# Kernel optimization log

Measured on AMD Instinct MI355X. Metric: run time of the kernel, lower is better.

The kernel has to match this reference:

```python
import jax, jax.numpy as jnp
import numpy as np

D_MODEL = 1024
D_Q = 1024
D_V = 1024


def setup_inputs() -> dict:
    key = jax.random.key(0)
    k0, k1, k2, k3 = jax.random.split(key, 4)
    embedding_word = jax.random.normal(k0, (4, 2048, D_MODEL), dtype=jnp.float32)
    # nn.Linear weights are [out, in]; we store transposed [in, out] for x @ W
    s = 1.0 / np.sqrt(D_MODEL)
    w_q = jax.random.uniform(k1, (D_MODEL, D_Q), jnp.float32, -s, s)
    w_k = jax.random.uniform(k2, (D_MODEL, D_Q), jnp.float32, -s, s)
    w_v = jax.random.uniform(k3, (D_MODEL, D_V), jnp.float32, -s, s)
    return {"embedding_word": embedding_word, "w_q": w_q, "w_k": w_k, "w_v": w_v}


def reference(embedding_word, w_q, w_k, w_v):
    # q,k: [B,T,d_q]; v: [B,T,d_v]
    q = embedding_word @ w_q
    k = embedding_word @ w_k
    v = embedding_word @ w_v
    scores = jnp.einsum("btd,bsd->bts", q, k)  # [B,T,T]
    T = scores.shape[-1]
    causal = jnp.tril(jnp.ones((T, T), dtype=bool))  # True = keep
    masked = jnp.where(causal, scores, -jnp.inf)
    weights = jax.nn.softmax(masked / jnp.sqrt(jnp.float32(D_Q)), axis=-1)
    return jnp.einsum("bts,bsv->btv", weights, v)
```

## Files before the change

### kernel.cpp

```cpp
#include <hip/hip_runtime.h>
#include <cstdint>

typedef __bf16 bf16_t;
typedef __attribute__((ext_vector_type(8))) __bf16 bf16x8;
typedef __attribute__((ext_vector_type(4))) __bf16 bf16x4;
typedef __attribute__((ext_vector_type(4))) float f32x4;

#define AS1 __attribute__((address_space(1)))
#define AS3 __attribute__((address_space(3)))

template <typename OutT>
__global__ __launch_bounds__(256)
void gemm_nt(const bf16_t* __restrict__ A, const bf16_t* __restrict__ B,
             OutT* __restrict__ C, int K, int lda, int ldb, int ldc)
{
  const int bm = blockIdx.y, bn = blockIdx.x;
  const int m0 = bm * 128, n0 = bn * 128;

  __shared__ bf16_t As[2][128 * 64];
  __shared__ bf16_t Bs[2][128 * 64];

  const int tid = threadIdx.x;
  const int wave = tid >> 6, lane = tid & 63;
  const int lm = lane & 15, qd = lane >> 4;
  const int wm = (wave >> 1) * 64, wn = (wave & 1) * 64;

  const int rowl = lane >> 3;
  const int q = (lane & 7) ^ rowl;
  const bf16_t* Abase = A + (long)(m0 + wave * 8 + rowl) * lda + q * 8;
  const bf16_t* Bbase = B + (long)(n0 + wave * 8 + rowl) * ldb + q * 8;
  const int woff = wave * 512;

  auto stage = [&](int k0, int b) {
#pragma unroll
    for (int i = 0; i < 4; i++) {
      __builtin_amdgcn_global_load_lds((const AS1 void*)(Abase + (long)i * 32 * lda + k0),
                                       (AS3 void*)(As[b] + woff + i * 2048), 16, 0, 0);
      __builtin_amdgcn_global_load_lds((const AS1 void*)(Bbase + (long)i * 32 * ldb + k0),
                                       (AS3 void*)(Bs[b] + woff + i * 2048), 16, 0, 0);
    }
  };

  f32x4 acc[4][4] = {};

  stage(0, 0);
  int buf = 0;
  for (int k0 = 0; k0 < K; k0 += 64) {
    __syncthreads();
    if (k0 + 64 < K) stage(k0 + 64, buf ^ 1);
#pragma unroll
    for (int s = 0; s < 2; s++) {
      bf16x8 aF[4], bF[4];
#pragma unroll
      for (int i = 0; i < 4; i++) {
        const int r = wm + i * 16 + lm;
        aF[i] = *(const bf16x8*)&As[buf][r * 64 + (((s * 4 + qd) ^ (lm & 7)) << 3)];
      }
#pragma unroll
      for (int j = 0; j < 4; j++) {
        const int r = wn + j * 16 + lm;
        bF[j] = *(const bf16x8*)&Bs[buf][r * 64 + (((s * 4 + qd) ^ (lm & 7)) << 3)];
      }
#pragma unroll
      for (int i = 0; i < 4; i++)
#pragma unroll
        for (int j = 0; j < 4; j++)
          acc[i][j] = __builtin_amdgcn_mfma_f32_16x16x32_bf16(aF[i], bF[j], acc[i][j], 0, 0, 0);
    }
    buf ^= 1;
  }

#pragma unroll
  for (int i = 0; i < 4; i++) {
    const int row = m0 + wm + i * 16 + qd * 4;
#pragma unroll
    for (int j = 0; j < 4; j++) {
      const int col = n0 + wn + j * 16 + lm;
#pragma unroll
      for (int r = 0; r < 4; r++)
        C[(long)(row + r) * ldc + col] = (OutT)acc[i][j][r];
    }
  }
}

template <typename OutT>
__global__ __launch_bounds__(256)
void gemm_ntc(const bf16_t* __restrict__ A, const bf16_t* __restrict__ B,
              OutT* __restrict__ C, int K, int lda, int ldb, int ldc,
              long sA, long sB, long sC, int causal, int kLimit)
{
  int bm = blockIdx.y;
  const int bn = blockIdx.x;
  if (kLimit) bm = gridDim.y - 1 - bm;
  if (causal && bn > bm) return;
  A += (long)blockIdx.z * sA;
  B += (long)blockIdx.z * sB;
  C += (long)blockIdx.z * sC;
  const int m0 = bm * 128, n0 = bn * 128;
  int Keff = K;
  if (kLimit) { const int kl = (bm + 1) * 128; if (kl < Keff) Keff = kl; }

  __shared__ bf16_t As[2][128 * 64];
  __shared__ bf16_t Bs[2][128 * 64];

  const int tid = threadIdx.x;
  const int wave = tid >> 6, lane = tid & 63;
  const int lm = lane & 15, qd = lane >> 4;
  const int wm = (wave >> 1) * 64, wn = (wave & 1) * 64;

  const int rowl = lane >> 3;
  const int q = (lane & 7) ^ rowl;
  const bf16_t* Abase = A + (long)(m0 + wave * 8 + rowl) * lda + q * 8;
  const bf16_t* Bbase = B + (long)(n0 + wave * 8 + rowl) * ldb + q * 8;
  const int woff = wave * 512;

  auto stage = [&](int k0, int b) {
#pragma unroll
    for (int i = 0; i < 4; i++) {
      __builtin_amdgcn_global_load_lds((const AS1 void*)(Abase + (long)i * 32 * lda + k0),
                                       (AS3 void*)(As[b] + woff + i * 2048), 16, 0, 0);
      __builtin_amdgcn_global_load_lds((const AS1 void*)(Bbase + (long)i * 32 * ldb + k0),
                                       (AS3 void*)(Bs[b] + woff + i * 2048), 16, 0, 0);
    }
  };

  f32x4 acc[4][4] = {};

  stage(0, 0);
  int buf = 0;
  for (int k0 = 0; k0 < Keff; k0 += 64) {
    __syncthreads();
    if (k0 + 64 < Keff) stage(k0 + 64, buf ^ 1);
#pragma unroll
    for (int s = 0; s < 2; s++) {
      bf16x8 aF[4], bF[4];
#pragma unroll
      for (int i = 0; i < 4; i++) {
        const int r = wm + i * 16 + lm;
        aF[i] = *(const bf16x8*)&As[buf][r * 64 + (((s * 4 + qd) ^ (lm & 7)) << 3)];
      }
#pragma unroll
      for (int j = 0; j < 4; j++) {
        const int r = wn + j * 16 + lm;
        bF[j] = *(const bf16x8*)&Bs[buf][r * 64 + (((s * 4 + qd) ^ (lm & 7)) << 3)];
      }
#pragma unroll
      for (int i = 0; i < 4; i++)
#pragma unroll
        for (int j = 0; j < 4; j++)
          acc[i][j] = __builtin_amdgcn_mfma_f32_16x16x32_bf16(aF[i], bF[j], acc[i][j], 0, 0, 0);
    }
    buf ^= 1;
  }

#pragma unroll
  for (int i = 0; i < 4; i++) {
    const int row = m0 + wm + i * 16 + qd * 4;
#pragma unroll
    for (int j = 0; j < 4; j++) {
      const int col = n0 + wn + j * 16 + lm;
#pragma unroll
      for (int r = 0; r < 4; r++)
        C[(long)(row + r) * ldc + col] = (OutT)acc[i][j][r];
    }
  }
}

__global__ __launch_bounds__(256)
void prep(const float* __restrict__ X, bf16_t* __restrict__ Xb,
          const float* __restrict__ wq, const float* __restrict__ wk,
          const float* __restrict__ wv, bf16_t* __restrict__ WT)
{
  const int b = blockIdx.x;
  if (b < 8192) {
    const int i = b * 256 + threadIdx.x;
    const float4 f = ((const float4*)X)[i];
    bf16x4 o = {(bf16_t)f.x, (bf16_t)f.y, (bf16_t)f.z, (bf16_t)f.w};
    ((bf16x4*)Xb)[i] = o;
    return;
  }
  const int wid = b - 8192;
  const int z = wid >> 10;
  const int t = wid & 1023;
  const int tix = t & 31, tiy = t >> 5;
  const float* W = (z == 0) ? wq : (z == 1) ? wk : wv;
  bf16_t* O = WT + (long)z * 1024 * 1024;

  __shared__ float tile[32][33];
  const int x = threadIdx.x & 31, y0 = threadIdx.x >> 5;
#pragma unroll
  for (int r = 0; r < 4; r++) {
    const int y = y0 + r * 8;
    tile[y][x] = W[(long)(tiy * 32 + y) * 1024 + (tix * 32 + x)];
  }
  __syncthreads();
#pragma unroll
  for (int r = 0; r < 4; r++) {
    const int y = y0 + r * 8;
    O[(long)(tix * 32 + y) * 1024 + (tiy * 32 + x)] = (bf16_t)tile[x][y];
  }
}

__global__ __launch_bounds__(256)
void softmax_causal(bf16_t* __restrict__ S)
{
  const int row = blockIdx.x;
  const int t = row & 2047;
  const int kend = ((t >> 7) + 1) << 7;
  bf16_t* Sr = S + (long)row * 2048;
  const int base = threadIdx.x * 8;

  uint4 u = {0, 0, 0, 0};
  if (base <= t) u = *(const uint4*)(Sr + base);
  const unsigned short* up = (const unsigned short*)&u;
  float v[8];
  float m = -3.0e38f;
#pragma unroll
  for (int j = 0; j < 8; j++) {
    const float x = __uint_as_float(((unsigned)up[j]) << 16);
    v[j] = (base + j <= t) ? x : -3.0e38f;
    m = fmaxf(m, v[j]);
  }
#pragma unroll
  for (int off = 32; off > 0; off >>= 1) m = fmaxf(m, __shfl_xor(m, off));
  __shared__ float redm[4], redl[4];
  const int wave = threadIdx.x >> 6, lane = threadIdx.x & 63;
  if (lane == 0) redm[wave] = m;
  __syncthreads();
  m = fmaxf(fmaxf(redm[0], redm[1]), fmaxf(redm[2], redm[3]));

  float p[8], l = 0.f;
#pragma unroll
  for (int j = 0; j < 8; j++) {
    p[j] = (base + j <= t) ? __expf((v[j] - m) * 0.03125f) : 0.f;
    l += p[j];
  }
#pragma unroll
  for (int off = 32; off > 0; off >>= 1) l += __shfl_xor(l, off);
  if (lane == 0) redl[wave] = l;
  __syncthreads();
  l = (redl[0] + redl[1]) + (redl[2] + redl[3]);
  const float rl = 1.0f / l;

  if (base < kend) {
    uint4 w;
    unsigned* wp = (unsigned*)&w;
#pragma unroll
    for (int h = 0; h < 4; h++) {
      bf16_t a = (bf16_t)(p[2 * h] * rl);
      bf16_t b = (bf16_t)(p[2 * h + 1] * rl);
      wp[h] = (unsigned)__builtin_bit_cast(unsigned short, a) |
              ((unsigned)__builtin_bit_cast(unsigned short, b) << 16);
    }
    *(uint4*)(Sr + base) = w;
  }
}

extern "C" void kernel_launch(void* const* d_in, const int* in_sizes, int n_in,
                              void* d_out, int out_size, void* d_ws, size_t ws_size,
                              hipStream_t stream)
{
  const float* X  = (const float*)d_in[0];
  const float* Wq = (const float*)d_in[1];
  const float* Wk = (const float*)d_in[2];
  const float* Wv = (const float*)d_in[3];
  float* out = (float*)d_out;

  char* p = (char*)d_ws;
  bf16_t* QK = (bf16_t*)p;  p += (size_t)8192 * 2048 * 2;
  bf16_t* VT = (bf16_t*)p;  p += (size_t)1024 * 8192 * 2;
  bf16_t* WT = (bf16_t*)p;  p += (size_t)3072 * 1024 * 2;
  bf16_t* Xb = (bf16_t*)p;
  bf16_t* S  = (bf16_t*)p;

  prep<<<8192 + 3072, 256, 0, stream>>>(X, Xb, Wq, Wk, Wv, WT);
  gemm_nt<bf16_t><<<dim3(16, 64), 256, 0, stream>>>(
      Xb, WT, QK, 1024, 1024, 1024, 2048);
  gemm_nt<bf16_t><<<dim3(64, 8), 256, 0, stream>>>(
      WT + (long)2048 * 1024, Xb, VT, 1024, 1024, 1024, 8192);
  gemm_ntc<bf16_t><<<dim3(16, 16, 4), 256, 0, stream>>>(
      QK, QK + 1024, S, 1024, 2048, 2048, 2048,
      (long)2048 * 2048, (long)2048 * 2048, (long)2048 * 2048, 1, 0);
  softmax_causal<<<8192, 256, 0, stream>>>(S);
  gemm_ntc<float><<<dim3(8, 16, 4), 256, 0, stream>>>(
      S, VT, out, 2048, 2048, 8192, 1024,
      (long)2048 * 2048, 2048, (long)2048 * 1024, 0, 1);
}
```

Measured before the change: 248.7 us.

## Replace 128x128 GEMMs with 256x256 8-wave ping-pong pipelined GEMM

Replaces both GEMM kernels with a single 256x256-tile kernel that runs 512 threads (8 waves). Its K loop is split into four MFMA phases, with LDS fragment reads and async global->LDS loads interleaved between them, separated by explicit barriers and guarded by s_setprio. The larger tile is meant to raise arithmetic intensity and hide load latency behind MFMA work. The causal block granularity grows to 256, so the softmax kend changes to match and more masked work runs near the diagonal. Grids shrink sharply (e.g. 128 or 256 blocks), which risks underfilling the CUs and adds heavy register pressure from the 8x4 accumulator array.

```diff
diff --git a/kernel.cpp b/kernel.cpp
--- a/kernel.cpp
+++ b/kernel.cpp
@@ -9,85 +9,45 @@
 #define AS1 __attribute__((address_space(1)))
 #define AS3 __attribute__((address_space(3)))
 
+
+#define READ_AQ(slot, bb, qidx)                                                \
+  _Pragma("unroll")                                                            \
+  for (int il = 0; il < 2; il++)                                               \
+    _Pragma("unroll")                                                          \
+    for (int s2 = 0; s2 < 2; s2++) {                                           \
+      const int r_ = wr * 128 + ((qidx) * 2 + il) * 16 + lm;                   \
+      aQ[slot][il * 2 + s2] =                                                  \
+        *(const bf16x8*)&As[bb][r_ * 64 + (((s2 * 4 + qd) ^ (lm & 7)) << 3)];  \
+    }
+
+#define READ_B(pi_, bb)                                                        \
+  _Pragma("unroll")                                                            \
+  for (int j = 0; j < 4; j++)                                                  \
+    _Pragma("unroll")                                                          \
+    for (int s2 = 0; s2 < 2; s2++) {                                           \
+      const int r_ = wc * 64 + j * 16 + lm;                                    \
+      bS[pi_][j * 2 + s2] =                                                    \
+        *(const bf16x8*)&Bs[bb][r_ * 64 + (((s2 * 4 + qd) ^ (lm & 7)) << 3)];  \
+    }
+
+#define MFMA_PH(p, slot, pi_)                                                  \
+  __builtin_amdgcn_s_setprio(1);                                               \
+  _Pragma("unroll")                                                            \
+  for (int il = 0; il < 2; il++)                                               \
+    _Pragma("unroll")                                                          \
+    for (int j = 0; j < 4; j++)                                                \
+      _Pragma("unroll")                                                        \
+      for (int s2 = 0; s2 < 2; s2++)                                           \
+        acc[(p) * 2 + il][j] = __builtin_amdgcn_mfma_f32_16x16x32_bf16(        \
+            aQ[slot][il * 2 + s2], bS[pi_][j * 2 + s2],                        \
+            acc[(p) * 2 + il][j], 0, 0, 0);                                    \
+  __builtin_amdgcn_s_setprio(0);
+
 template <typename OutT>
-__global__ __launch_bounds__(256)
-void gemm_nt(const bf16_t* __restrict__ A, const bf16_t* __restrict__ B,
-             OutT* __restrict__ C, int K, int lda, int ldb, int ldc)
-{
-  const int bm = blockIdx.y, bn = blockIdx.x;
-  const int m0 = bm * 128, n0 = bn * 128;
-
-  __shared__ bf16_t As[2][128 * 64];
-  __shared__ bf16_t Bs[2][128 * 64];
-
-  const int tid = threadIdx.x;
-  const int wave = tid >> 6, lane = tid & 63;
-  const int lm = lane & 15, qd = lane >> 4;
-  const int wm = (wave >> 1) * 64, wn = (wave & 1) * 64;
-
-  const int rowl = lane >> 3;
-  const int q = (lane & 7) ^ rowl;
-  const bf16_t* Abase = A + (long)(m0 + wave * 8 + rowl) * lda + q * 8;
-  const bf16_t* Bbase = B + (long)(n0 + wave * 8 + rowl) * ldb + q * 8;
-  const int woff = wave * 512;
-
-  auto stage = [&](int k0, int b) {
-#pragma unroll
-    for (int i = 0; i < 4; i++) {
-      __builtin_amdgcn_global_load_lds((const AS1 void*)(Abase + (long)i * 32 * lda + k0),
-                                       (AS3 void*)(As[b] + woff + i * 2048), 16, 0, 0);
-      __builtin_amdgcn_global_load_lds((const AS1 void*)(Bbase + (long)i * 32 * ldb + k0),
-                                       (AS3 void*)(Bs[b] + woff + i * 2048), 16, 0, 0);
-    }
-  };
-
-  f32x4 acc[4][4] = {};
-
-  stage(0, 0);
-  int buf = 0;
-  for (int k0 = 0; k0 < K; k0 += 64) {
-    __syncthreads();
-    if (k0 + 64 < K) stage(k0 + 64, buf ^ 1);
-#pragma unroll
-    for (int s = 0; s < 2; s++) {
-      bf16x8 aF[4], bF[4];
-#pragma unroll
-      for (int i = 0; i < 4; i++) {
-        const int r = wm + i * 16 + lm;
-        aF[i] = *(const bf16x8*)&As[buf][r * 64 + (((s * 4 + qd) ^ (lm & 7)) << 3)];
-      }
-#pragma unroll
-      for (int j = 0; j < 4; j++) {
-        const int r = wn + j * 16 + lm;
-        bF[j] = *(const bf16x8*)&Bs[buf][r * 64 + (((s * 4 + qd) ^ (lm & 7)) << 3)];
-      }
-#pragma unroll
-      for (int i = 0; i < 4; i++)
-#pragma unroll
-        for (int j = 0; j < 4; j++)
-          acc[i][j] = __builtin_amdgcn_mfma_f32_16x16x32_bf16(aF[i], bF[j], acc[i][j], 0, 0, 0);
-    }
-    buf ^= 1;
-  }
-
-#pragma unroll
-  for (int i = 0; i < 4; i++) {
-    const int row = m0 + wm + i * 16 + qd * 4;
-#pragma unroll
-    for (int j = 0; j < 4; j++) {
-      const int col = n0 + wn + j * 16 + lm;
-#pragma unroll
-      for (int r = 0; r < 4; r++)
-        C[(long)(row + r) * ldc + col] = (OutT)acc[i][j][r];
-    }
-  }
-}
-
-template <typename OutT>
-__global__ __launch_bounds__(256)
-void gemm_ntc(const bf16_t* __restrict__ A, const bf16_t* __restrict__ B,
-              OutT* __restrict__ C, int K, int lda, int ldb, int ldc,
-              long sA, long sB, long sC, int causal, int kLimit)
+__global__ __launch_bounds__(512, 2)
+void gemm256(const bf16_t* __restrict__ A, const bf16_t* __restrict__ B,
+             OutT* __restrict__ C, int K, int lda, int ldb, int ldc,
+             long sA, long sB, long sC, int causal, int kLimit)
 {
   int bm = blockIdx.y;
   const int bn = blockIdx.x;
@@ -96,69 +56,90 @@
   A += (long)blockIdx.z * sA;
   B += (long)blockIdx.z * sB;
   C += (long)blockIdx.z * sC;
-  const int m0 = bm * 128, n0 = bn * 128;
+  const int m0 = bm * 256, n0 = bn * 256;
   int Keff = K;
-  if (kLimit) { const int kl = (bm + 1) * 128; if (kl < Keff) Keff = kl; }
-
-  __shared__ bf16_t As[2][128 * 64];
-  __shared__ bf16_t Bs[2][128 * 64];
+  if (kLimit) { const int kl = (bm + 1) * 256; if (kl < Keff) Keff = kl; }
+
+  __shared__ bf16_t As[2][256 * 64];
+  __shared__ bf16_t Bs[2][256 * 64];
 
   const int tid = threadIdx.x;
   const int wave = tid >> 6, lane = tid & 63;
   const int lm = lane & 15, qd = lane >> 4;
-  const int wm = (wave >> 1) * 64, wn = (wave & 1) * 64;
-
+  const int wr = wave >> 2, wc = wave & 3;
   const int rowl = lane >> 3;
   const int q = (lane & 7) ^ rowl;
   const bf16_t* Abase = A + (long)(m0 + wave * 8 + rowl) * lda + q * 8;
   const bf16_t* Bbase = B + (long)(n0 + wave * 8 + rowl) * ldb + q * 8;
   const int woff = wave * 512;
 
-  auto stage = [&](int k0, int b) {
-#pragma unroll
-    for (int i = 0; i < 4; i++) {
-      __builtin_amdgcn_global_load_lds((const AS1 void*)(Abase + (long)i * 32 * lda + k0),
-                                       (AS3 void*)(As[b] + woff + i * 2048), 16, 0, 0);
-      __builtin_amdgcn_global_load_lds((const AS1 void*)(Bbase + (long)i * 32 * ldb + k0),
-                                       (AS3 void*)(Bs[b] + woff + i * 2048), 16, 0, 0);
-    }
+  auto stgA = [&](int kt, int b, int h) {
+#pragma unroll
+    for (int i = 0; i < 2; i++)
+      __builtin_amdgcn_global_load_lds(
+          (const AS1 void*)(Abase + (long)(h * 128 + i * 64) * lda + kt),
+          (AS3 void*)(As[b] + h * 8192 + i * 4096 + woff), 16, 0, 0);
   };
-
-  f32x4 acc[4][4] = {};
-
-  stage(0, 0);
-  int buf = 0;
-  for (int k0 = 0; k0 < Keff; k0 += 64) {
-    __syncthreads();
-    if (k0 + 64 < Keff) stage(k0 + 64, buf ^ 1);
-#pragma unroll
-    for (int s = 0; s < 2; s++) {
-      bf16x8 aF[4], bF[4];
-#pragma unroll
-      for (int i = 0; i < 4; i++) {
-        const int r = wm + i * 16 + lm;
-        aF[i] = *(const bf16x8*)&As[buf][r * 64 + (((s * 4 + qd) ^ (lm & 7)) << 3)];
-      }
-#pragma unroll
-      for (int j = 0; j < 4; j++) {
-        const int r = wn + j * 16 + lm;
-        bF[j] = *(const bf16x8*)&Bs[buf][r * 64 + (((s * 4 + qd) ^ (lm & 7)) << 3)];
-      }
-#pragma unroll
-      for (int i = 0; i < 4; i++)
-#pragma unroll
-        for (int j = 0; j < 4; j++)
-          acc[i][j] = __builtin_amdgcn_mfma_f32_16x16x32_bf16(aF[i], bF[j], acc[i][j], 0, 0, 0);
-    }
-    buf ^= 1;
-  }
-
-#pragma unroll
-  for (int i = 0; i < 4; i++) {
-    const int row = m0 + wm + i * 16 + qd * 4;
+  auto stgB = [&](int kt, int b, int h) {
+#pragma unroll
+    for (int i = 0; i < 2; i++)
+      __builtin_amdgcn_global_load_lds(
+          (const AS1 void*)(Bbase + (long)(h * 128 + i * 64) * ldb + kt),
+          (AS3 void*)(Bs[b] + h * 8192 + i * 4096 + woff), 16, 0, 0);
+  };
+
+  f32x4 acc[8][4] = {};
+  bf16x8 aQ[2][4];
+  bf16x8 bS[2][8];
+
+  stgB(0, 0, 0);  stgB(0, 0, 1);  stgA(0, 0, 0);  stgA(0, 0, 1);
+  stgB(64, 1, 0); stgB(64, 1, 1); stgA(64, 1, 0); stgA(64, 1, 1);
+  asm volatile("s_waitcnt vmcnt(8)" ::: "memory");
+  __builtin_amdgcn_s_barrier();
+  READ_B(0, 0);
+  READ_AQ(0, 0, 0);
+  __builtin_amdgcn_s_barrier();
+
+  for (int k0 = 0; k0 < Keff; k0 += 128) {
+#pragma unroll
+    for (int tt = 0; tt < 2; tt++) {
+      const int kk = k0 + tt * 64;
+      const bool stg = (kk + 128 < Keff);
+      const bool nxt = (kk + 64 < Keff);
+      READ_AQ(1, tt, 1);
+      if (stg) stgB(kk + 128, tt, 0);
+      __builtin_amdgcn_s_barrier();
+      __builtin_amdgcn_sched_barrier(0);
+      MFMA_PH(0, 0, tt);
+      __builtin_amdgcn_s_barrier();
+      READ_AQ(0, tt, 2);
+      if (stg) stgB(kk + 128, tt, 1);
+      __builtin_amdgcn_s_barrier();
+      __builtin_amdgcn_sched_barrier(0);
+      MFMA_PH(1, 1, tt);
+      __builtin_amdgcn_s_barrier();
+      READ_AQ(1, tt, 3);
+      if (stg) asm volatile("s_waitcnt vmcnt(4)" ::: "memory");
+      else     asm volatile("s_waitcnt vmcnt(0)" ::: "memory");
+      __builtin_amdgcn_s_barrier();
+      __builtin_amdgcn_sched_barrier(0);
+      MFMA_PH(2, 0, tt);
+      __builtin_amdgcn_s_barrier();
+      if (nxt) { READ_B(tt ^ 1, tt ^ 1); READ_AQ(0, tt ^ 1, 0); }
+      if (stg) { stgA(kk + 128, tt, 0); stgA(kk + 128, tt, 1); }
+      __builtin_amdgcn_s_barrier();
+      __builtin_amdgcn_sched_barrier(0);
+      MFMA_PH(3, 1, tt);
+      __builtin_amdgcn_s_barrier();
+    }
+  }
+
+#pragma unroll
+  for (int i = 0; i < 8; i++) {
+    const int row = m0 + wr * 128 + i * 16 + qd * 4;
 #pragma unroll
     for (int j = 0; j < 4; j++) {
-      const int col = n0 + wn + j * 16 + lm;
+      const int col = n0 + wc * 64 + j * 16 + lm;
 #pragma unroll
       for (int r = 0; r < 4; r++)
         C[(long)(row + r) * ldc + col] = (OutT)acc[i][j][r];
@@ -206,7 +187,7 @@
 {
   const int row = blockIdx.x;
   const int t = row & 2047;
-  const int kend = ((t >> 7) + 1) << 7;
+  const int kend = ((t >> 8) + 1) << 8;
   bf16_t* Sr = S + (long)row * 2048;
   const int base = threadIdx.x * 8;
 
@@ -274,15 +255,15 @@
   bf16_t* S  = (bf16_t*)p;
 
   prep<<<8192 + 3072, 256, 0, stream>>>(X, Xb, Wq, Wk, Wv, WT);
-  gemm_nt<bf16_t><<<dim3(16, 64), 256, 0, stream>>>(
-      Xb, WT, QK, 1024, 1024, 1024, 2048);
-  gemm_nt<bf16_t><<<dim3(64, 8), 256, 0, stream>>>(
-      WT + (long)2048 * 1024, Xb, VT, 1024, 1024, 1024, 8192);
-  gemm_ntc<bf16_t><<<dim3(16, 16, 4), 256, 0, stream>>>(
+  gemm256<bf16_t><<<dim3(8, 32, 1), 512, 0, stream>>>(
+      Xb, WT, QK, 1024, 1024, 1024, 2048, 0, 0, 0, 0, 0);
+  gemm256<bf16_t><<<dim3(32, 4, 1), 512, 0, stream>>>(
+      WT + (long)2048 * 1024, Xb, VT, 1024, 1024, 1024, 8192, 0, 0, 0, 0, 0);
+  gemm256<bf16_t><<<dim3(8, 8, 4), 512, 0, stream>>>(
       QK, QK + 1024, S, 1024, 2048, 2048, 2048,
       (long)2048 * 2048, (long)2048 * 2048, (long)2048 * 2048, 1, 0);
   softmax_causal<<<8192, 256, 0, stream>>>(S);
-  gemm_ntc<float><<<dim3(8, 16, 4), 256, 0, stream>>>(
+  gemm256<float><<<dim3(4, 8, 4), 512, 0, stream>>>(
       S, VT, out, 2048, 2048, 8192, 1024,
       (long)2048 * 2048, 2048, (long)2048 * 1024, 0, 1);
 }
```

Measured after the change: 289.2 us. 16.3% more time.

## Add 256x256-tile 8-wave GEMM with phased pipeline for Q/K projection

Applied to the files above, without the earlier changes.

Adds a new 512-thread GEMM kernel that computes 256x256 output tiles, splitting each K-step into four phases that interleave LDS fragment reads, async global-to-LDS staging of the next tiles and MFMA bursts under raised priority. It replaces the 128x128 kernel for the fused Q/K projection only. The larger tile raises arithmetic intensity and cuts global traffic per FLOP. In exchange it uses 128 KB of LDS and many accumulator registers per thread, and launches only 256 blocks, which may leave some CUs idle.

```diff
diff --git a/kernel.cpp b/kernel.cpp
--- a/kernel.cpp
+++ b/kernel.cpp
@@ -166,6 +166,123 @@
   }
 }
 
+template <typename OutT>
+__global__ __launch_bounds__(512, 2)
+void gemm256(const bf16_t* __restrict__ A, const bf16_t* __restrict__ B,
+             OutT* __restrict__ C, int K, int lda, int ldb, int ldc)
+{
+  const int bm = blockIdx.y, bn = blockIdx.x;
+  const int m0 = bm * 256, n0 = bn * 256;
+
+  __shared__ bf16_t As[2][256 * 64];
+  __shared__ bf16_t Bs[2][256 * 64];
+
+  const int tid = threadIdx.x;
+  const int wave = tid >> 6, lane = tid & 63;
+  const int lm = lane & 15, qd = lane >> 4;
+  const int wr = wave >> 2, wc = wave & 3;
+  const int wch = wc >> 1, wcl = wc & 1;
+  const int rowl = lane >> 3;
+  const int q = (lane & 7) ^ rowl;
+  const int woff = wave * 512;
+
+  auto stgAc = [&](int kt, int b, int c) {
+    const int grow = m0 + ((c & 1) << 7) + ((c >> 1) << 6) + wave * 8 + rowl;
+    __builtin_amdgcn_global_load_lds(
+        (const AS1 void*)(A + (long)grow * lda + q * 8 + kt),
+        (AS3 void*)(As[b] + c * 4096 + woff), 16, 0, 0);
+  };
+  auto stgBc = [&](int kt, int b, int c) {
+    const int gn = n0 + ((c & 1) << 7) + ((wave >> 2) << 6) + ((c >> 1) << 5) +
+                   (wave & 3) * 8 + rowl;
+    __builtin_amdgcn_global_load_lds(
+        (const AS1 void*)(B + (long)gn * ldb + q * 8 + kt),
+        (AS3 void*)(Bs[b] + c * 4096 + woff), 16, 0, 0);
+  };
+
+  f32x4 acc[8][4] = {};
+
+#define PHASE256(p, d, dn, kk, stg1, stg2)                                     \
+  {                                                                            \
+    constexpr int mp = (p) >> 1, np = (p) & 1;                                 \
+    bf16x8 aF[4][2], bF[2][2];                                                 \
+    _Pragma("unroll")                                                          \
+    for (int mi = 0; mi < 4; mi++)                                             \
+      _Pragma("unroll")                                                        \
+      for (int s2 = 0; s2 < 2; s2++) {                                         \
+        const int r_ = (wr + 2 * mp) * 64 + mi * 16 + lm;                      \
+        aF[mi][s2] =                                                           \
+          *(const bf16x8*)&As[d][r_ * 64 + (((s2 * 4 + qd) ^ (lm & 7)) << 3)]; \
+      }                                                                        \
+    _Pragma("unroll")                                                          \
+    for (int nj = 0; nj < 2; nj++)                                             \
+      _Pragma("unroll")                                                        \
+      for (int s2 = 0; s2 < 2; s2++) {                                         \
+        const int r_ = (np * 2 + wch) * 64 + wcl * 32 + nj * 16 + lm;          \
+        bF[nj][s2] =                                                           \
+          *(const bf16x8*)&Bs[d][r_ * 64 + (((s2 * 4 + qd) ^ (lm & 7)) << 3)]; \
+      }                                                                        \
+    if ((p) == 0 && (stg1)) { stgAc((kk) + 64, dn, 2); stgAc((kk) + 64, dn, 3); } \
+    if ((p) == 1 && (stg1)) { stgBc((kk) + 64, dn, 2); stgBc((kk) + 64, dn, 3); } \
+    if ((p) == 2 && (stg2)) { stgAc((kk) + 128, d, 0); stgAc((kk) + 128, d, 1); } \
+    if ((p) == 3 && (stg2)) { stgBc((kk) + 128, d, 0); stgBc((kk) + 128, d, 1); } \
+    if ((p) == 3) {                                                            \
+      if (stg2) asm volatile("s_waitcnt vmcnt(4)" ::: "memory");               \
+      else      asm volatile("s_waitcnt vmcnt(0)" ::: "memory");               \
+    }                                                                          \
+    __builtin_amdgcn_s_barrier();                                              \
+    asm volatile("s_waitcnt lgkmcnt(0)" ::: "memory");                         \
+    __builtin_amdgcn_sched_barrier(0);                                         \
+    __builtin_amdgcn_s_setprio(1);                                             \
+    _Pragma("unroll")                                                          \
+    for (int mi = 0; mi < 4; mi++)                                             \
+      _Pragma("unroll")                                                        \
+      for (int nj = 0; nj < 2; nj++)                                           \
+        _Pragma("unroll")                                                      \
+        for (int s2 = 0; s2 < 2; s2++)                                         \
+          acc[mp * 4 + mi][np * 2 + nj] =                                      \
+              __builtin_amdgcn_mfma_f32_16x16x32_bf16(                         \
+                  aF[mi][s2], bF[nj][s2], acc[mp * 4 + mi][np * 2 + nj],       \
+                  0, 0, 0);                                                    \
+    __builtin_amdgcn_s_setprio(0);                                             \
+    __builtin_amdgcn_s_barrier();                                              \
+  }
+
+  stgAc(0, 0, 0); stgAc(0, 0, 1); stgAc(0, 0, 2); stgAc(0, 0, 3);
+  stgBc(0, 0, 0); stgBc(0, 0, 1); stgBc(0, 0, 2); stgBc(0, 0, 3);
+  stgAc(64, 1, 0); stgAc(64, 1, 1);
+  stgBc(64, 1, 0); stgBc(64, 1, 1);
+  asm volatile("s_waitcnt vmcnt(4)" ::: "memory");
+  __builtin_amdgcn_s_barrier();
+
+  for (int kk = 0; kk < K; kk += 128) {
+    const bool s1a = (kk + 64  < K);
+    const bool s2a = (kk + 128 < K);
+    const bool s2b = (kk + 192 < K);
+    PHASE256(0, 0, 1, kk, s1a, s2a)
+    PHASE256(1, 0, 1, kk, s1a, s2a)
+    PHASE256(2, 0, 1, kk, s1a, s2a)
+    PHASE256(3, 0, 1, kk, s1a, s2a)
+    PHASE256(0, 1, 0, kk + 64, s2a, s2b)
+    PHASE256(1, 1, 0, kk + 64, s2a, s2b)
+    PHASE256(2, 1, 0, kk + 64, s2a, s2b)
+    PHASE256(3, 1, 0, kk + 64, s2a, s2b)
+  }
+#undef PHASE256
+
+#pragma unroll
+  for (int i = 0; i < 8; i++) {
+    const int row = m0 + wr * 128 + i * 16 + qd * 4;
+#pragma unroll
+    for (int j = 0; j < 4; j++) {
+      const int col = n0 + wc * 64 + j * 16 + lm;
+#pragma unroll
+      for (int r = 0; r < 4; r++)
+        C[(long)(row + r) * ldc + col] = (OutT)acc[i][j][r];
+    }
+  }
+}
+
 __global__ __launch_bounds__(256)
 void prep(const float* __restrict__ X, bf16_t* __restrict__ Xb,
           const float* __restrict__ wq, const float* __restrict__ wk,
@@ -274,7 +391,7 @@
   bf16_t* S  = (bf16_t*)p;
 
   prep<<<8192 + 3072, 256, 0, stream>>>(X, Xb, Wq, Wk, Wv, WT);
-  gemm_nt<bf16_t><<<dim3(16, 64), 256, 0, stream>>>(
+  gemm256<bf16_t><<<dim3(8, 32), 512, 0, stream>>>(
       Xb, WT, QK, 1024, 1024, 1024, 2048);
   gemm_nt<bf16_t><<<dim3(64, 8), 256, 0, stream>>>(
       WT + (long)2048 * 1024, Xb, VT, 1024, 1024, 1024, 8192);
```

Result: no change. 249.8 us (+0.4%).

## Merge QKV GEMMs into one launch and use a triangular grid for scores

Applied to the files above, without the earlier changes.

The separate Q/K and V projection GEMM launches become a single kernel that picks the operands from a flat block index, which drops one launch and lets the two GEMMs share the GPU. The causal QK^T GEMM now launches only the 136 lower-triangle tiles per batch, mapped with a sqrt-based index, instead of launching 256 tiles and returning early from half of them. The fp32-to-bf16 conversion in prep switches to a grid-stride loop over fewer blocks. The GEMM body is moved into a shared device function.

```diff
diff --git a/kernel.cpp b/kernel.cpp
--- a/kernel.cpp
+++ b/kernel.cpp
@@ -1,5 +1,6 @@
 #include <hip/hip_runtime.h>
 #include <cstdint>
+#include <cmath>
 
 typedef __bf16 bf16_t;
 typedef __attribute__((ext_vector_type(8))) __bf16 bf16x8;
@@ -10,16 +11,11 @@
 #define AS3 __attribute__((address_space(3)))
 
 template <typename OutT>
-__global__ __launch_bounds__(256)
-void gemm_nt(const bf16_t* __restrict__ A, const bf16_t* __restrict__ B,
-             OutT* __restrict__ C, int K, int lda, int ldb, int ldc)
-{
-  const int bm = blockIdx.y, bn = blockIdx.x;
-  const int m0 = bm * 128, n0 = bn * 128;
-
-  __shared__ bf16_t As[2][128 * 64];
-  __shared__ bf16_t Bs[2][128 * 64];
-
+__device__ __forceinline__
+void gemm128_body(const bf16_t* A, const bf16_t* B, OutT* C,
+                  int K, int lda, int ldb, int ldc, int m0, int n0,
+                  bf16_t (*As)[128 * 64], bf16_t (*Bs)[128 * 64])
+{
   const int tid = threadIdx.x;
   const int wave = tid >> 6, lane = tid & 63;
   const int lm = lane & 15, qd = lane >> 4;
@@ -83,87 +79,56 @@
   }
 }
 
-template <typename OutT>
+__global__ __launch_bounds__(256)
+void gemm_qkv(const bf16_t* __restrict__ Xb, const bf16_t* __restrict__ WT,
+              bf16_t* __restrict__ QK, bf16_t* __restrict__ VT)
+{
+  __shared__ bf16_t As[2][128 * 64];
+  __shared__ bf16_t Bs[2][128 * 64];
+
+  const int id = blockIdx.x;
+  const bf16_t *Ap, *Bp;
+  bf16_t* Cp;
+  int bm, bn, ldc;
+  if (id < 1024) {
+    bm = id & 63; bn = id >> 6;
+    Ap = Xb; Bp = WT; Cp = QK; ldc = 2048;
+  } else {
+    const int j = id - 1024;
+    bn = j & 63; bm = j >> 6;
+    Ap = WT + (long)2048 * 1024; Bp = Xb; Cp = VT; ldc = 8192;
+  }
+  gemm128_body<bf16_t>(Ap, Bp, Cp, 1024, 1024, 1024, ldc,
+                       bm * 128, bn * 128, As, Bs);
+}
+
+template <typename OutT, int TAG, int TRI>
 __global__ __launch_bounds__(256)
 void gemm_ntc(const bf16_t* __restrict__ A, const bf16_t* __restrict__ B,
               OutT* __restrict__ C, int K, int lda, int ldb, int ldc,
-              long sA, long sB, long sC, int causal, int kLimit)
-{
-  int bm = blockIdx.y;
-  const int bn = blockIdx.x;
-  if (kLimit) bm = gridDim.y - 1 - bm;
-  if (causal && bn > bm) return;
-  A += (long)blockIdx.z * sA;
-  B += (long)blockIdx.z * sB;
-  C += (long)blockIdx.z * sC;
-  const int m0 = bm * 128, n0 = bn * 128;
+              long sA, long sB, long sC, int kLimit)
+{
+  int bm, bn;
+  if (TRI) {
+    const int j = blockIdx.x;
+    bm = (int)((sqrtf(8.f * j + 1.f) - 1.f) * 0.5f);
+    if (bm * (bm + 1) / 2 > j) bm--;
+    bn = j - bm * (bm + 1) / 2;
+  } else {
+    bm = blockIdx.y;
+    bn = blockIdx.x;
+    if (kLimit) bm = gridDim.y - 1 - bm;
+  }
+  const bf16_t* Ab = A + (long)blockIdx.z * sA;
+  const bf16_t* Bb = B + (long)blockIdx.z * sB;
+  OutT* Cb = C + (long)blockIdx.z * sC;
   int Keff = K;
-  if (kLimit) { const int kl = (bm + 1) * 128; if (kl < Keff) Keff = kl; }
+  if (!TRI && kLimit) { const int kl = (bm + 1) * 128; if (kl < Keff) Keff = kl; }
 
   __shared__ bf16_t As[2][128 * 64];
   __shared__ bf16_t Bs[2][128 * 64];
-
-  const int tid = threadIdx.x;
-  const int wave = tid >> 6, lane = tid & 63;
-  const int lm = lane & 15, qd = lane >> 4;
-  const int wm = (wave >> 1) * 64, wn = (wave & 1) * 64;
-
-  const int rowl = lane >> 3;
-  const int q = (lane & 7) ^ rowl;
-  const bf16_t* Abase = A + (long)(m0 + wave * 8 + rowl) * lda + q * 8;
-  const bf16_t* Bbase = B + (long)(n0 + wave * 8 + rowl) * ldb + q * 8;
-  const int woff = wave * 512;
-
-  auto stage = [&](int k0, int b) {
-#pragma unroll
-    for (int i = 0; i < 4; i++) {
-      __builtin_amdgcn_global_load_lds((const AS1 void*)(Abase + (long)i * 32 * lda + k0),
-                                       (AS3 void*)(As[b] + woff + i * 2048), 16, 0, 0);
-      __builtin_amdgcn_global_load_lds((const AS1 void*)(Bbase + (long)i * 32 * ldb + k0),
-                                       (AS3 void*)(Bs[b] + woff + i * 2048), 16, 0, 0);
-    }
-  };
-
-  f32x4 acc[4][4] = {};
-
-  stage(0, 0);
-  int buf = 0;
-  for (int k0 = 0; k0 < Keff; k0 += 64) {
-    __syncthreads();
-    if (k0 + 64 < Keff) stage(k0 + 64, buf ^ 1);
-#pragma unroll
-    for (int s = 0; s < 2; s++) {
-      bf16x8 aF[4], bF[4];
-#pragma unroll
-      for (int i = 0; i < 4; i++) {
-        const int r = wm + i * 16 + lm;
-        aF[i] = *(const bf16x8*)&As[buf][r * 64 + (((s * 4 + qd) ^ (lm & 7)) << 3)];
-      }
-#pragma unroll
-      for (int j = 0; j < 4; j++) {
-        const int r = wn + j * 16 + lm;
-        bF[j] = *(const bf16x8*)&Bs[buf][r * 64 + (((s * 4 + qd) ^ (lm & 7)) << 3)];
-      }
-#pragma unroll
-      for (int i = 0; i < 4; i++)
-#pragma unroll
-        for (int j = 0; j < 4; j++)
-          acc[i][j] = __builtin_amdgcn_mfma_f32_16x16x32_bf16(aF[i], bF[j], acc[i][j], 0, 0, 0);
-    }
-    buf ^= 1;
-  }
-
-#pragma unroll
-  for (int i = 0; i < 4; i++) {
-    const int row = m0 + wm + i * 16 + qd * 4;
-#pragma unroll
-    for (int j = 0; j < 4; j++) {
-      const int col = n0 + wn + j * 16 + lm;
-#pragma unroll
-      for (int r = 0; r < 4; r++)
-        C[(long)(row + r) * ldc + col] = (OutT)acc[i][j][r];
-    }
-  }
+  gemm128_body<OutT>(Ab, Bb, Cb, Keff, lda, ldb, ldc,
+                     bm * 128, bn * 128, As, Bs);
 }
 
 __global__ __launch_bounds__(256)
@@ -172,14 +137,17 @@
           const float* __restrict__ wv, bf16_t* __restrict__ WT)
 {
   const int b = blockIdx.x;
-  if (b < 8192) {
-    const int i = b * 256 + threadIdx.x;
-    const float4 f = ((const float4*)X)[i];
-    bf16x4 o = {(bf16_t)f.x, (bf16_t)f.y, (bf16_t)f.z, (bf16_t)f.w};
-    ((bf16x4*)Xb)[i] = o;
+  if (b < 2048) {
+    const int N4 = 8192 * 1024 / 4;
+    const int stride = 2048 * 256;
+    for (int i = b * 256 + threadIdx.x; i < N4; i += stride) {
+      const float4 f = ((const float4*)X)[i];
+      bf16x4 o = {(bf16_t)f.x, (bf16_t)f.y, (bf16_t)f.z, (bf16_t)f.w};
+      ((bf16x4*)Xb)[i] = o;
+    }
     return;
   }
-  const int wid = b - 8192;
+  const int wid = b - 2048;
   const int z = wid >> 10;
   const int t = wid & 1023;
   const int tix = t & 31, tiy = t >> 5;
@@ -273,16 +241,13 @@
   bf16_t* Xb = (bf16_t*)p;
   bf16_t* S  = (bf16_t*)p;
 
-  prep<<<8192 + 3072, 256, 0, stream>>>(X, Xb, Wq, Wk, Wv, WT);
-  gemm_nt<bf16_t><<<dim3(16, 64), 256, 0, stream>>>(
-      Xb, WT, QK, 1024, 1024, 1024, 2048);
-  gemm_nt<bf16_t><<<dim3(64, 8), 256, 0, stream>>>(
-      WT + (long)2048 * 1024, Xb, VT, 1024, 1024, 1024, 8192);
-  gemm_ntc<bf16_t><<<dim3(16, 16, 4), 256, 0, stream>>>(
+  prep<<<2048 + 3072, 256, 0, stream>>>(X, Xb, Wq, Wk, Wv, WT);
+  gemm_qkv<<<1536, 256, 0, stream>>>(Xb, WT, QK, VT);
+  gemm_ntc<bf16_t, 4, 1><<<dim3(136, 1, 4), 256, 0, stream>>>(
       QK, QK + 1024, S, 1024, 2048, 2048, 2048,
-      (long)2048 * 2048, (long)2048 * 2048, (long)2048 * 2048, 1, 0);
+      (long)2048 * 2048, (long)2048 * 2048, (long)2048 * 2048, 0);
   softmax_causal<<<8192, 256, 0, stream>>>(S);
-  gemm_ntc<float><<<dim3(8, 16, 4), 256, 0, stream>>>(
+  gemm_ntc<float, 6, 0><<<dim3(8, 16, 4), 256, 0, stream>>>(
       S, VT, out, 2048, 2048, 8192, 1024,
-      (long)2048 * 2048, 2048, (long)2048 * 1024, 0, 1);
-}
+      (long)2048 * 2048, 2048, (long)2048 * 1024, 1);
+}
```

After: 273.6 us. 1.1x slower.
